# Kernel optimization log

Hardware: AMD Instinct MI355X
Metric: run time of the kernel (lower is better)

## Reference

```python
import jax, jax.numpy as jnp
import numpy as np

N_NODES = 100000
N_EDGES = 800000
C = 64        # in_channels == out_channels
H = 4         # num_heads
LN_EPS = 1e-5
SM_EPS = 1e-8


def setup_inputs() -> dict:
    key = jax.random.key(0)
    ks = jax.random.split(key, 8)
    return {
        "x": jax.random.normal(ks[0], (N_NODES, C), dtype=jnp.float32),
        "edge_index": jax.random.randint(ks[1], (2, N_EDGES), 0, N_NODES, dtype=jnp.int64),
        "edge_time": jax.random.uniform(ks[2], (N_EDGES,), dtype=jnp.float32),
        "current_time": 1,
        "W_w": jax.random.normal(ks[3], (C, C), dtype=jnp.float32) * (1.0 / np.sqrt(C)),
        "W_b": jnp.zeros((C,), dtype=jnp.float32),
        "attn_w": jax.random.normal(ks[4], (2 * C, H), dtype=jnp.float32) * (1.0 / np.sqrt(2 * C)),
        "attn_b": jnp.zeros((H,), dtype=jnp.float32),
        "decay_rate": jnp.full((1,), 0.1, dtype=jnp.float32),
        "proj_w": jax.random.normal(ks[5], (C * H, C), dtype=jnp.float32) * (1.0 / np.sqrt(C * H)),
        "proj_b": jnp.zeros((C,), dtype=jnp.float32),
        "ln_g": jnp.ones((C,), dtype=jnp.float32),
        "ln_b": jnp.zeros((C,), dtype=jnp.float32),
    }


def reference(x, edge_index, edge_time, current_time, W_w, W_b, attn_w, attn_b,
              decay_rate, proj_w, proj_b, ln_g, ln_b):
    num_nodes = x.shape[0]
    src, dst = edge_index[0], edge_index[1]

    # relation-specific transform (same Linear applied to src and dst node sets)
    h = x @ W_w + W_b                       # (N, C)
    h_src = h[src]                          # (E, C) gather
    h_dst = h[dst]                          # (E, C) gather

    # attention: Linear(2C -> H) + LeakyReLU(0.2)
    logits = h_src @ attn_w[:C] + h_dst @ attn_w[C:] + attn_b   # (E, H)
    scores = jax.nn.leaky_relu(logits, negative_slope=0.2)

    # temporal decay: exp(-softplus(lambda) * delta_t), multiplied pre-softmax
    delta_t = jnp.float32(current_time) - edge_time             # (E,)
    lam = jax.nn.softplus(decay_rate[0])
    scores = scores * jnp.exp(-lam * delta_t)[:, None]

    # segmented (per-destination) softmax over incoming edges
    smax = jax.ops.segment_max(scores, dst, num_segments=num_nodes)   # (N, H)
    e = jnp.exp(scores - smax[dst])                                   # (E, H)
    ssum = jax.ops.segment_sum(e, dst, num_segments=num_nodes)        # (N, H)
    attn = e / (ssum[dst] + SM_EPS)                                   # (E, H)

    # per-edge messages (E, C, H) -> (E, C*H), scatter-add to destinations
    msg = (h_src[:, :, None] * attn[:, None, :]).reshape(-1, C * H)
    agg = jax.ops.segment_sum(msg, dst, num_segments=num_nodes)       # (N, C*H)

    # single edge type -> mean over 1 message is identity
    out = agg @ proj_w + proj_b                                       # (N, C)
    # dropout p=0 (eval) -> identity; residual + LayerNorm + ReLU
    z = out + x
    mu = jnp.mean(z, axis=-1, keepdims=True)
    var = jnp.mean(jnp.square(z - mu), axis=-1, keepdims=True)
    y = ln_g * (z - mu) * jax.lax.rsqrt(var + LN_EPS) + ln_b
    return jax.nn.relu(y)
```

## Files before the change

### kernel.cpp

```cpp
#include <hip/hip_runtime.h>


typedef __attribute__((ext_vector_type(8))) short bf16x8;
typedef __attribute__((ext_vector_type(4))) float f32x4;

__device__ __forceinline__ unsigned short f2bf(float f) {
  unsigned int u = __float_as_uint(f);
  u += 0x7FFFu + ((u >> 16) & 1u);
  return (unsigned short)(u >> 16);
}
__device__ __forceinline__ float bf2f(unsigned short s) {
  return __uint_as_float(((unsigned int)s) << 16);
}

#define FMA4(P, S, R) { P.x = fmaf(S, R.x, P.x); P.y = fmaf(S, R.y, P.y); \
                        P.z = fmaf(S, R.z, P.z); P.w = fmaf(S, R.w, P.w); }

__global__ __launch_bounds__(64) void k_hn(const float* __restrict__ x,
    const float* __restrict__ Ww, const float* __restrict__ Wb,
    const float* __restrict__ attn_w,
    unsigned short* __restrict__ h16, float4* __restrict__ u,
    float4* __restrict__ v, int N)
{
  const int n = blockIdx.x * 64 + threadIdx.x;
  const bool valid = (n < N);
  const int nc = valid ? n : (N - 1);

  float o[64];
  #pragma unroll
  for (int c = 0; c < 64; ++c) o[c] = Wb[c];

  const float* xr = x + (size_t)nc * 64;
  for (int ch = 0; ch < 16; ++ch) {
    float4 xv = *(const float4*)(xr + ch * 4);
    float a[4] = {xv.x, xv.y, xv.z, xv.w};
    #pragma unroll
    for (int kk = 0; kk < 4; ++kk) {
      const float* Wr = Ww + (size_t)(ch * 4 + kk) * 64;
      #pragma unroll
      for (int c = 0; c < 64; ++c)
        o[c] = fmaf(a[kk], Wr[c], o[c]);
    }
  }

  float4 uu = make_float4(0.f, 0.f, 0.f, 0.f);
  float4 vv = make_float4(0.f, 0.f, 0.f, 0.f);
  const float4* aw = (const float4*)attn_w;
  #pragma unroll
  for (int c = 0; c < 64; ++c) {
    float4 r1 = aw[c];
    float4 r2 = aw[64 + c];
    FMA4(uu, o[c], r1);
    FMA4(vv, o[c], r2);
  }

  if (valid) {
    unsigned int* hr = (unsigned int*)(h16 + (size_t)n * 64);
    #pragma unroll
    for (int i = 0; i < 8; ++i) {
      uint4 w;
      w.x = (unsigned int)f2bf(o[i*8+0]) | ((unsigned int)f2bf(o[i*8+1]) << 16);
      w.y = (unsigned int)f2bf(o[i*8+2]) | ((unsigned int)f2bf(o[i*8+3]) << 16);
      w.z = (unsigned int)f2bf(o[i*8+4]) | ((unsigned int)f2bf(o[i*8+5]) << 16);
      w.w = (unsigned int)f2bf(o[i*8+6]) | ((unsigned int)f2bf(o[i*8+7]) << 16);
      *(uint4*)(hr + i * 4) = w;
    }
    u[n] = uu;
    v[n] = vv;
  }
}

__global__ __launch_bounds__(256) void k_score(const float4* __restrict__ u,
    const float4* __restrict__ v,
    const int* __restrict__ ei, const float* __restrict__ et,
    const int* __restrict__ ctime, const float* __restrict__ drate,
    const float* __restrict__ attn_b, float4* __restrict__ est,
    int* __restrict__ deg, int* __restrict__ rank, int E)
{
  int e = blockIdx.x * 256 + threadIdx.x;
  if (e >= E) return;
  const int src = ei[e];
  const int dst = ei[E + e];
  rank[e] = atomicAdd(&deg[dst], 1);
  const float4 us = u[src];
  const float4 vd = v[dst];
  const float4 ab = *(const float4*)attn_b;
  const float lam = log1pf(__expf(drate[0]));
  const float w = __expf(-lam * ((float)ctime[0] - et[e]));

  float4 o; float t;
  t = us.x + vd.x + ab.x; t = (t > 0.f ? t : 0.2f * t) * w; o.x = __expf(t);
  t = us.y + vd.y + ab.y; t = (t > 0.f ? t : 0.2f * t) * w; o.y = __expf(t);
  t = us.z + vd.z + ab.z; t = (t > 0.f ? t : 0.2f * t) * w; o.z = __expf(t);
  t = us.w + vd.w + ab.w; t = (t > 0.f ? t : 0.2f * t) * w; o.w = __expf(t);
  est[e] = o;
}

__global__ __launch_bounds__(256) void scan1(const int* __restrict__ deg,
    int* __restrict__ offs, int* __restrict__ bsums, int N)
{
  int i = blockIdx.x * 256 + threadIdx.x;
  int lane = threadIdx.x & 63;
  int w = threadIdx.x >> 6;
  int v = (i < N) ? deg[i] : 0;
  int s = v;
  #pragma unroll
  for (int d = 1; d < 64; d <<= 1) {
    int t = __shfl_up(s, d, 64);
    if (lane >= d) s += t;
  }
  __shared__ int wsum[4];
  if (lane == 63) wsum[w] = s;
  __syncthreads();
  int add = 0;
  if (w > 0) add += wsum[0];
  if (w > 1) add += wsum[1];
  if (w > 2) add += wsum[2];
  if (i < N) offs[i] = s - v + add;
  if (threadIdx.x == 255) bsums[blockIdx.x] = wsum[0] + wsum[1] + wsum[2] + wsum[3];
}

__global__ __launch_bounds__(512) void scan2(int* bsums, int NB)
{
  __shared__ int lds[512];
  int t = threadIdx.x;
  int v = (t < NB) ? bsums[t] : 0;
  lds[t] = v;
  __syncthreads();
  for (int s = 1; s < 512; s <<= 1) {
    int a = (t >= s) ? lds[t - s] : 0;
    __syncthreads();
    lds[t] += a;
    __syncthreads();
  }
  if (t < NB) bsums[t] = lds[t] - v;
}

__global__ __launch_bounds__(256) void k_fill(const int* __restrict__ ei,
    const int* __restrict__ offs, const int* __restrict__ bsums,
    const int* __restrict__ rank, const float4* __restrict__ est,
    int* __restrict__ csr_src, float4* __restrict__ csr_es, int E)
{
  int e = blockIdx.x * 256 + threadIdx.x;
  if (e >= E) return;
  int d = ei[E + e];
  int pos = offs[d] + bsums[d >> 8] + rank[e];
  csr_src[pos] = ei[e];
  csr_es[pos] = est[e];
}

__global__ __launch_bounds__(256) void k_agg(const unsigned short* __restrict__ h16,
    const int* __restrict__ csr_src, const float4* __restrict__ csr_es,
    const int* __restrict__ offs, const int* __restrict__ bsums,
    unsigned short* __restrict__ agg, int N, int E)
{
  const int c = threadIdx.x & 63;
  const int wid = blockIdx.x * 4 + (threadIdx.x >> 6);
  const int wstride = gridDim.x * 4;

  for (int n0 = wid; n0 < N; n0 += wstride) {
    const int n = __builtin_amdgcn_readfirstlane(n0);
    const int p0 = offs[n] + bsums[n >> 8];
    const int p1 = (n + 1 < N) ? (offs[n + 1] + bsums[(n + 1) >> 8]) : E;
    const int nf = (p1 - p0) & ~3;

    float acc0 = 0.f, acc1 = 0.f, acc2 = 0.f, acc3 = 0.f;
    float den0 = 0.f, den1 = 0.f, den2 = 0.f, den3 = 0.f;

    int4   sA = make_int4(0, 0, 0, 0);
    float4 eA0, eA1, eA2, eA3;
    float  gA0 = 0.f, gA1 = 0.f, gA2 = 0.f, gA3 = 0.f;
    if (nf) {
      sA = *(const int4*)(csr_src + p0);
      eA0 = csr_es[p0];     eA1 = csr_es[p0 + 1];
      eA2 = csr_es[p0 + 2]; eA3 = csr_es[p0 + 3];
      gA0 = bf2f(h16[(size_t)sA.x * 64 + c]);
      gA1 = bf2f(h16[(size_t)sA.y * 64 + c]);
      gA2 = bf2f(h16[(size_t)sA.z * 64 + c]);
      gA3 = bf2f(h16[(size_t)sA.w * 64 + c]);
    }
    for (int p = p0; p < p0 + nf; p += 4) {
      int4 sB; float4 eB0, eB1, eB2, eB3;
      float gB0, gB1, gB2, gB3;
      const bool more = (p + 4 < p0 + nf);
      if (more) {
        sB = *(const int4*)(csr_src + p + 4);
        eB0 = csr_es[p + 4]; eB1 = csr_es[p + 5];
        eB2 = csr_es[p + 6]; eB3 = csr_es[p + 7];
        gB0 = bf2f(h16[(size_t)sB.x * 64 + c]);
        gB1 = bf2f(h16[(size_t)sB.y * 64 + c]);
        gB2 = bf2f(h16[(size_t)sB.z * 64 + c]);
        gB3 = bf2f(h16[(size_t)sB.w * 64 + c]);
      }
      den0 += (eA0.x + eA1.x) + (eA2.x + eA3.x);
      den1 += (eA0.y + eA1.y) + (eA2.y + eA3.y);
      den2 += (eA0.z + eA1.z) + (eA2.z + eA3.z);
      den3 += (eA0.w + eA1.w) + (eA2.w + eA3.w);
      acc0 = fmaf(eA0.x, gA0, fmaf(eA1.x, gA1, fmaf(eA2.x, gA2, fmaf(eA3.x, gA3, acc0))));
      acc1 = fmaf(eA0.y, gA0, fmaf(eA1.y, gA1, fmaf(eA2.y, gA2, fmaf(eA3.y, gA3, acc1))));
      acc2 = fmaf(eA0.z, gA0, fmaf(eA1.z, gA1, fmaf(eA2.z, gA2, fmaf(eA3.z, gA3, acc2))));
      acc3 = fmaf(eA0.w, gA0, fmaf(eA1.w, gA1, fmaf(eA2.w, gA2, fmaf(eA3.w, gA3, acc3))));
      if (more) {
        eA0 = eB0; eA1 = eB1; eA2 = eB2; eA3 = eB3;
        gA0 = gB0; gA1 = gB1; gA2 = gB2; gA3 = gB3;
      }
    }
    for (int p = p0 + nf; p < p1; ++p) {
      int s = csr_src[p];
      float4 ev = csr_es[p];
      float g = bf2f(h16[(size_t)s * 64 + c]);
      den0 += ev.x; den1 += ev.y; den2 += ev.z; den3 += ev.w;
      acc0 = fmaf(ev.x, g, acc0);
      acc1 = fmaf(ev.y, g, acc1);
      acc2 = fmaf(ev.z, g, acc2);
      acc3 = fmaf(ev.w, g, acc3);
    }
    ushort4 o;
    o.x = f2bf(acc0 / (den0 + 1e-8f));
    o.y = f2bf(acc1 / (den1 + 1e-8f));
    o.z = f2bf(acc2 / (den2 + 1e-8f));
    o.w = f2bf(acc3 / (den3 + 1e-8f));
    *(ushort4*)(agg + (size_t)n * 256 + c * 4) = o;
  }
}

__global__ __launch_bounds__(256) void k_pw(const float* __restrict__ Pw,
    unsigned short* __restrict__ Bf)
{
  int i = blockIdx.x * 256 + threadIdx.x;
  int j    = i & 7;
  int lane = (i >> 3) & 63;
  int cb   = (i >> 9) & 3;
  int ks   = i >> 11;
  int k    = ks * 32 + (lane >> 4) * 8 + j;
  int colg = cb * 16 + (lane & 15);
  Bf[i] = f2bf(Pw[(size_t)k * 64 + colg]);
}

__global__ __launch_bounds__(256) void k_projm(const unsigned short* __restrict__ agg,
    const unsigned short* __restrict__ Bf, const float* __restrict__ x,
    const float* __restrict__ Pb,
    const float* __restrict__ lg, const float* __restrict__ lb,
    float* __restrict__ out, int N)
{
  const int lane = threadIdx.x & 63;
  const int wv = threadIdx.x >> 6;
  const int nt = blockIdx.x * 4 + wv;
  if (nt * 16 >= N) return;
  const int col  = lane & 15;
  const int quad = lane >> 4;
  const int base = nt * 16;

  int na = base + col; if (na >= N) na = N - 1;
  const unsigned short* aptr = agg + (size_t)na * 256 + quad * 8;

  f32x4 acc0 = {0.f, 0.f, 0.f, 0.f};
  f32x4 acc1 = {0.f, 0.f, 0.f, 0.f};
  f32x4 acc2 = {0.f, 0.f, 0.f, 0.f};
  f32x4 acc3 = {0.f, 0.f, 0.f, 0.f};

  #pragma unroll
  for (int ks = 0; ks < 8; ++ks) {
    bf16x8 av = *(const bf16x8*)(aptr + ks * 32);
    bf16x8 b0 = *(const bf16x8*)(Bf + ((size_t)(ks * 4 + 0) * 64 + lane) * 8);
    bf16x8 b1 = *(const bf16x8*)(Bf + ((size_t)(ks * 4 + 1) * 64 + lane) * 8);
    bf16x8 b2 = *(const bf16x8*)(Bf + ((size_t)(ks * 4 + 2) * 64 + lane) * 8);
    bf16x8 b3 = *(const bf16x8*)(Bf + ((size_t)(ks * 4 + 3) * 64 + lane) * 8);
    acc0 = __builtin_amdgcn_mfma_f32_16x16x32_bf16(av, b0, acc0, 0, 0, 0);
    acc1 = __builtin_amdgcn_mfma_f32_16x16x32_bf16(av, b1, acc1, 0, 0, 0);
    acc2 = __builtin_amdgcn_mfma_f32_16x16x32_bf16(av, b2, acc2, 0, 0, 0);
    acc3 = __builtin_amdgcn_mfma_f32_16x16x32_bf16(av, b3, acc3, 0, 0, 0);
  }

  const float pb0 = Pb[col], pb1 = Pb[16 + col], pb2 = Pb[32 + col], pb3 = Pb[48 + col];
  float v[4][4];
  #pragma unroll
  for (int r = 0; r < 4; ++r) {
    int node = base + quad * 4 + r; if (node >= N) node = N - 1;
    const float* xr = x + (size_t)node * 64;
    v[0][r] = acc0[r] + pb0 + xr[col];
    v[1][r] = acc1[r] + pb1 + xr[16 + col];
    v[2][r] = acc2[r] + pb2 + xr[32 + col];
    v[3][r] = acc3[r] + pb3 + xr[48 + col];
  }

  float mu[4], inv[4];
  #pragma unroll
  for (int r = 0; r < 4; ++r) {
    float s = (v[0][r] + v[1][r]) + (v[2][r] + v[3][r]);
    s += __shfl_xor(s, 1, 64); s += __shfl_xor(s, 2, 64);
    s += __shfl_xor(s, 4, 64); s += __shfl_xor(s, 8, 64);
    mu[r] = s * 0.015625f;
  }
  #pragma unroll
  for (int r = 0; r < 4; ++r) {
    float d0 = v[0][r] - mu[r], d1 = v[1][r] - mu[r];
    float d2 = v[2][r] - mu[r], d3 = v[3][r] - mu[r];
    float s = fmaf(d0, d0, d1 * d1) + fmaf(d2, d2, d3 * d3);
    s += __shfl_xor(s, 1, 64); s += __shfl_xor(s, 2, 64);
    s += __shfl_xor(s, 4, 64); s += __shfl_xor(s, 8, 64);
    inv[r] = rsqrtf(s * 0.015625f + 1e-5f);
  }

  const float lg0 = lg[col], lg1 = lg[16 + col], lg2 = lg[32 + col], lg3 = lg[48 + col];
  const float lb0 = lb[col], lb1 = lb[16 + col], lb2 = lb[32 + col], lb3 = lb[48 + col];
  #pragma unroll
  for (int r = 0; r < 4; ++r) {
    int node = base + quad * 4 + r;
    if (node < N) {
      float* orow = out + (size_t)node * 64;
      orow[col]      = fmaxf(fmaf(lg0 * (v[0][r] - mu[r]), inv[r], lb0), 0.f);
      orow[16 + col] = fmaxf(fmaf(lg1 * (v[1][r] - mu[r]), inv[r], lb1), 0.f);
      orow[32 + col] = fmaxf(fmaf(lg2 * (v[2][r] - mu[r]), inv[r], lb2), 0.f);
      orow[48 + col] = fmaxf(fmaf(lg3 * (v[3][r] - mu[r]), inv[r], lb3), 0.f);
    }
  }
}

extern "C" void kernel_launch(void* const* d_in, const int* in_sizes, int n_in,
                              void* d_out, int out_size, void* d_ws, size_t ws_size,
                              hipStream_t stream)
{
  const float* x  = (const float*)d_in[0];
  const int*   ei = (const int*)d_in[1];
  const float* et = (const float*)d_in[2];
  const int*   ct = (const int*)d_in[3];
  const float* Ww = (const float*)d_in[4];
  const float* Wb = (const float*)d_in[5];
  const float* aw = (const float*)d_in[6];
  const float* ab = (const float*)d_in[7];
  const float* dr = (const float*)d_in[8];
  const float* Pw = (const float*)d_in[9];
  const float* Pb = (const float*)d_in[10];
  const float* lg = (const float*)d_in[11];
  const float* lb = (const float*)d_in[12];
  float* out = (float*)d_out;

  const int N = in_sizes[0] / 64;
  const int E = in_sizes[2];

  char* ws = (char*)d_ws;
  size_t off = 0;
  auto take = [&](size_t bytes) -> char* {
    char* p = ws + off;
    off = (off + bytes + 255) & ~(size_t)255;
    return p;
  };
  unsigned short* h16 = (unsigned short*)take((size_t)N * 64 * 2);
  int*    deg    = (int*)take((size_t)N * 4);
  int*    offs   = (int*)take((size_t)N * 4);
  int*    bsums  = (int*)take(512 * 4);
  int*    rank   = (int*)take((size_t)E * 4);
  float4* est    = (float4*)take((size_t)E * 16);
  int*    csr_src= (int*)take((size_t)E * 4);
  float4* csr_es = (float4*)take((size_t)E * 16);
  unsigned short* agg = (unsigned short*)take((size_t)N * 256 * 2);
  float4* u      = (float4*)take((size_t)N * 16);
  float4* v      = (float4*)take((size_t)N * 16);
  unsigned short* Bf = (unsigned short*)take(16384 * 2);

  hipMemsetAsync(deg, 0, (size_t)N * 4, stream);

  k_pw<<<64, 256, 0, stream>>>(Pw, Bf);
  k_hn<<<(N + 63) / 64, 64, 0, stream>>>(x, Ww, Wb, aw, h16, u, v, N);
  k_score<<<(E + 255) / 256, 256, 0, stream>>>(u, v, ei, et, ct, dr, ab, est, deg, rank, E);
  const int NB = (N + 255) / 256;
  scan1<<<NB, 256, 0, stream>>>(deg, offs, bsums, N);
  scan2<<<1, 512, 0, stream>>>(bsums, NB);
  k_fill<<<(E + 255) / 256, 256, 0, stream>>>(ei, offs, bsums, rank, est, csr_src, csr_es, E);
  k_agg<<<2048, 256, 0, stream>>>(h16, csr_src, csr_es, offs, bsums, agg, N, E);
  const int NT = (N + 15) / 16;
  k_projm<<<(NT + 3) / 4, 256, 0, stream>>>(agg, Bf, x, Pb, lg, lb, out, N);
}
```

Before: 281.5 us.

## Fuse score computation into CSR fill and aggregation into projection+LayerNorm

Splits the old score kernel so a lightweight kernel only computes degrees and ranks. The edge-score computation moves into the CSR fill kernel, which removes the intermediate per-edge score buffer and its round trip through memory. The per-destination aggregation is fused with the MFMA projection, residual and LayerNorm: each block stages 16 aggregated rows in LDS as bf16, and the four waves then each compute 16 output columns, with LayerNorm statistics reduced through shared memory. This removes the N×256 bf16 agg buffer write and read, at the cost of a fixed one-node-per-wave mapping instead of grid-stride load balancing, plus extra barriers.

Result: slower. 322.8 us (+14.7%).

```diff
diff --git a/kernel.cpp b/kernel.cpp
--- a/kernel.cpp
+++ b/kernel.cpp
@@ -11,6 +11,9 @@
 }
 __device__ __forceinline__ float bf2f(unsigned short s) {
   return __uint_as_float(((unsigned int)s) << 16);
+}
+__device__ __forceinline__ unsigned int pk(float a, float b) {
+  return (unsigned int)f2bf(a) | ((unsigned int)f2bf(b) << 16);
 }
 
 #define FMA4(P, S, R) { P.x = fmaf(S, R.x, P.x); P.y = fmaf(S, R.y, P.y); \
@@ -59,10 +62,10 @@
     #pragma unroll
     for (int i = 0; i < 8; ++i) {
       uint4 w;
-      w.x = (unsigned int)f2bf(o[i*8+0]) | ((unsigned int)f2bf(o[i*8+1]) << 16);
-      w.y = (unsigned int)f2bf(o[i*8+2]) | ((unsigned int)f2bf(o[i*8+3]) << 16);
-      w.z = (unsigned int)f2bf(o[i*8+4]) | ((unsigned int)f2bf(o[i*8+5]) << 16);
-      w.w = (unsigned int)f2bf(o[i*8+6]) | ((unsigned int)f2bf(o[i*8+7]) << 16);
+      w.x = pk(o[i*8+0], o[i*8+1]);
+      w.y = pk(o[i*8+2], o[i*8+3]);
+      w.z = pk(o[i*8+4], o[i*8+5]);
+      w.w = pk(o[i*8+6], o[i*8+7]);
       *(uint4*)(hr + i * 4) = w;
     }
     u[n] = uu;
@@ -70,30 +73,11 @@
   }
 }
 
-__global__ __launch_bounds__(256) void k_score(const float4* __restrict__ u,
-    const float4* __restrict__ v,
-    const int* __restrict__ ei, const float* __restrict__ et,
-    const int* __restrict__ ctime, const float* __restrict__ drate,
-    const float* __restrict__ attn_b, float4* __restrict__ est,
+__global__ __launch_bounds__(256) void k_deg(const int* __restrict__ ei,
     int* __restrict__ deg, int* __restrict__ rank, int E)
 {
   int e = blockIdx.x * 256 + threadIdx.x;
-  if (e >= E) return;
-  const int src = ei[e];
-  const int dst = ei[E + e];
-  rank[e] = atomicAdd(&deg[dst], 1);
-  const float4 us = u[src];
-  const float4 vd = v[dst];
-  const float4 ab = *(const float4*)attn_b;
-  const float lam = log1pf(__expf(drate[0]));
-  const float w = __expf(-lam * ((float)ctime[0] - et[e]));
-
-  float4 o; float t;
-  t = us.x + vd.x + ab.x; t = (t > 0.f ? t : 0.2f * t) * w; o.x = __expf(t);
-  t = us.y + vd.y + ab.y; t = (t > 0.f ? t : 0.2f * t) * w; o.y = __expf(t);
-  t = us.z + vd.z + ab.z; t = (t > 0.f ? t : 0.2f * t) * w; o.z = __expf(t);
-  t = us.w + vd.w + ab.w; t = (t > 0.f ? t : 0.2f * t) * w; o.w = __expf(t);
-  est[e] = o;
+  if (e < E) rank[e] = atomicAdd(&deg[ei[E + e]], 1);
 }
 
 __global__ __launch_bounds__(256) void scan1(const int* __restrict__ deg,
@@ -137,91 +121,32 @@
 }
 
 __global__ __launch_bounds__(256) void k_fill(const int* __restrict__ ei,
+    const float* __restrict__ et, const int* __restrict__ ctime,
+    const float* __restrict__ drate, const float4* __restrict__ u,
+    const float4* __restrict__ v, const float* __restrict__ attn_b,
     const int* __restrict__ offs, const int* __restrict__ bsums,
-    const int* __restrict__ rank, const float4* __restrict__ est,
+    const int* __restrict__ rank,
     int* __restrict__ csr_src, float4* __restrict__ csr_es, int E)
 {
   int e = blockIdx.x * 256 + threadIdx.x;
   if (e >= E) return;
-  int d = ei[E + e];
-  int pos = offs[d] + bsums[d >> 8] + rank[e];
-  csr_src[pos] = ei[e];
-  csr_es[pos] = est[e];
-}
-
-__global__ __launch_bounds__(256) void k_agg(const unsigned short* __restrict__ h16,
-    const int* __restrict__ csr_src, const float4* __restrict__ csr_es,
-    const int* __restrict__ offs, const int* __restrict__ bsums,
-    unsigned short* __restrict__ agg, int N, int E)
-{
-  const int c = threadIdx.x & 63;
-  const int wid = blockIdx.x * 4 + (threadIdx.x >> 6);
-  const int wstride = gridDim.x * 4;
-
-  for (int n0 = wid; n0 < N; n0 += wstride) {
-    const int n = __builtin_amdgcn_readfirstlane(n0);
-    const int p0 = offs[n] + bsums[n >> 8];
-    const int p1 = (n + 1 < N) ? (offs[n + 1] + bsums[(n + 1) >> 8]) : E;
-    const int nf = (p1 - p0) & ~3;
-
-    float acc0 = 0.f, acc1 = 0.f, acc2 = 0.f, acc3 = 0.f;
-    float den0 = 0.f, den1 = 0.f, den2 = 0.f, den3 = 0.f;
-
-    int4   sA = make_int4(0, 0, 0, 0);
-    float4 eA0, eA1, eA2, eA3;
-    float  gA0 = 0.f, gA1 = 0.f, gA2 = 0.f, gA3 = 0.f;
-    if (nf) {
-      sA = *(const int4*)(csr_src + p0);
-      eA0 = csr_es[p0];     eA1 = csr_es[p0 + 1];
-      eA2 = csr_es[p0 + 2]; eA3 = csr_es[p0 + 3];
-      gA0 = bf2f(h16[(size_t)sA.x * 64 + c]);
-      gA1 = bf2f(h16[(size_t)sA.y * 64 + c]);
-      gA2 = bf2f(h16[(size_t)sA.z * 64 + c]);
-      gA3 = bf2f(h16[(size_t)sA.w * 64 + c]);
-    }
-    for (int p = p0; p < p0 + nf; p += 4) {
-      int4 sB; float4 eB0, eB1, eB2, eB3;
-      float gB0, gB1, gB2, gB3;
-      const bool more = (p + 4 < p0 + nf);
-      if (more) {
-        sB = *(const int4*)(csr_src + p + 4);
-        eB0 = csr_es[p + 4]; eB1 = csr_es[p + 5];
-        eB2 = csr_es[p + 6]; eB3 = csr_es[p + 7];
-        gB0 = bf2f(h16[(size_t)sB.x * 64 + c]);
-        gB1 = bf2f(h16[(size_t)sB.y * 64 + c]);
-        gB2 = bf2f(h16[(size_t)sB.z * 64 + c]);
-        gB3 = bf2f(h16[(size_t)sB.w * 64 + c]);
-      }
-      den0 += (eA0.x + eA1.x) + (eA2.x + eA3.x);
-      den1 += (eA0.y + eA1.y) + (eA2.y + eA3.y);
-      den2 += (eA0.z + eA1.z) + (eA2.z + eA3.z);
-      den3 += (eA0.w + eA1.w) + (eA2.w + eA3.w);
-      acc0 = fmaf(eA0.x, gA0, fmaf(eA1.x, gA1, fmaf(eA2.x, gA2, fmaf(eA3.x, gA3, acc0))));
-      acc1 = fmaf(eA0.y, gA0, fmaf(eA1.y, gA1, fmaf(eA2.y, gA2, fmaf(eA3.y, gA3, acc1))));
-      acc2 = fmaf(eA0.z, gA0, fmaf(eA1.z, gA1, fmaf(eA2.z, gA2, fmaf(eA3.z, gA3, acc2))));
-      acc3 = fmaf(eA0.w, gA0, fmaf(eA1.w, gA1, fmaf(eA2.w, gA2, fmaf(eA3.w, gA3, acc3))));
-      if (more) {
-        eA0 = eB0; eA1 = eB1; eA2 = eB2; eA3 = eB3;
-        gA0 = gB0; gA1 = gB1; gA2 = gB2; gA3 = gB3;
-      }
-    }
-    for (int p = p0 + nf; p < p1; ++p) {
-      int s = csr_src[p];
-      float4 ev = csr_es[p];
-      float g = bf2f(h16[(size_t)s * 64 + c]);
-      den0 += ev.x; den1 += ev.y; den2 += ev.z; den3 += ev.w;
-      acc0 = fmaf(ev.x, g, acc0);
-      acc1 = fmaf(ev.y, g, acc1);
-      acc2 = fmaf(ev.z, g, acc2);
-      acc3 = fmaf(ev.w, g, acc3);
-    }
-    ushort4 o;
-    o.x = f2bf(acc0 / (den0 + 1e-8f));
-    o.y = f2bf(acc1 / (den1 + 1e-8f));
-    o.z = f2bf(acc2 / (den2 + 1e-8f));
-    o.w = f2bf(acc3 / (den3 + 1e-8f));
-    *(ushort4*)(agg + (size_t)n * 256 + c * 4) = o;
-  }
+  const int s = ei[e];
+  const int d = ei[E + e];
+  const float4 us = u[s];
+  const float4 vd = v[d];
+  const float4 ab = *(const float4*)attn_b;
+  const float lam = log1pf(__expf(drate[0]));
+  const float w = __expf(-lam * ((float)ctime[0] - et[e]));
+
+  float4 o; float t;
+  t = us.x + vd.x + ab.x; t = (t > 0.f ? t : 0.2f * t) * w; o.x = __expf(t);
+  t = us.y + vd.y + ab.y; t = (t > 0.f ? t : 0.2f * t) * w; o.y = __expf(t);
+  t = us.z + vd.z + ab.z; t = (t > 0.f ? t : 0.2f * t) * w; o.z = __expf(t);
+  t = us.w + vd.w + ab.w; t = (t > 0.f ? t : 0.2f * t) * w; o.w = __expf(t);
+
+  const int pos = offs[d] + bsums[d >> 8] + rank[e];
+  csr_src[pos] = s;
+  csr_es[pos] = o;
 }
 
 __global__ __launch_bounds__(256) void k_pw(const float* __restrict__ Pw,
@@ -237,83 +162,126 @@
   Bf[i] = f2bf(Pw[(size_t)k * 64 + colg]);
 }
 
-__global__ __launch_bounds__(256) void k_projm(const unsigned short* __restrict__ agg,
-    const unsigned short* __restrict__ Bf, const float* __restrict__ x,
-    const float* __restrict__ Pb,
+__global__ __launch_bounds__(256) void k_aggproj(
+    const unsigned short* __restrict__ h16,
+    const int* __restrict__ csr_src, const float4* __restrict__ csr_es,
+    const int* __restrict__ offs, const int* __restrict__ bsums,
+    const unsigned short* __restrict__ Bf,
+    const float* __restrict__ x, const float* __restrict__ Pb,
     const float* __restrict__ lg, const float* __restrict__ lb,
-    float* __restrict__ out, int N)
-{
+    float* __restrict__ out, int N, int E)
+{
+  __shared__ unsigned short At[16][264];
+  __shared__ float S1[16][4], S2[16][4];
+
   const int lane = threadIdx.x & 63;
   const int wv = threadIdx.x >> 6;
-  const int nt = blockIdx.x * 4 + wv;
-  if (nt * 16 >= N) return;
-  const int col  = lane & 15;
-  const int quad = lane >> 4;
-  const int base = nt * 16;
-
-  int na = base + col; if (na >= N) na = N - 1;
-  const unsigned short* aptr = agg + (size_t)na * 256 + quad * 8;
-
-  f32x4 acc0 = {0.f, 0.f, 0.f, 0.f};
-  f32x4 acc1 = {0.f, 0.f, 0.f, 0.f};
-  f32x4 acc2 = {0.f, 0.f, 0.f, 0.f};
-  f32x4 acc3 = {0.f, 0.f, 0.f, 0.f};
-
+  const int base = blockIdx.x * 16;
+  const int c = lane;
+
+  for (int i = 0; i < 4; ++i) {
+    const int row = wv * 4 + i;
+    const int n = base + row;
+    float acc0 = 0.f, acc1 = 0.f, acc2 = 0.f, acc3 = 0.f;
+    float den0 = 0.f, den1 = 0.f, den2 = 0.f, den3 = 0.f;
+    if (n < N) {
+      const int p0 = offs[n] + bsums[n >> 8];
+      const int p1 = (n + 1 < N) ? (offs[n + 1] + bsums[(n + 1) >> 8]) : E;
+      const int nf = (p1 - p0) & ~3;
+
+      int4   sA = make_int4(0, 0, 0, 0);
+      float4 eA0, eA1, eA2, eA3;
+      float  gA0 = 0.f, gA1 = 0.f, gA2 = 0.f, gA3 = 0.f;
+      if (nf) {
+        sA = *(const int4*)(csr_src + p0);
+        eA0 = csr_es[p0];     eA1 = csr_es[p0 + 1];
+        eA2 = csr_es[p0 + 2]; eA3 = csr_es[p0 + 3];
+        gA0 = bf2f(h16[(size_t)sA.x * 64 + c]);
+        gA1 = bf2f(h16[(size_t)sA.y * 64 + c]);
+        gA2 = bf2f(h16[(size_t)sA.z * 64 + c]);
+        gA3 = bf2f(h16[(size_t)sA.w * 64 + c]);
+      }
+      for (int p = p0; p < p0 + nf; p += 4) {
+        int4 sB; float4 eB0, eB1, eB2, eB3;
+        float gB0, gB1, gB2, gB3;
+        const bool more = (p + 4 < p0 + nf);
+        if (more) {
+          sB = *(const int4*)(csr_src + p + 4);
+          eB0 = csr_es[p + 4]; eB1 = csr_es[p + 5];
+          eB2 = csr_es[p + 6]; eB3 = csr_es[p + 7];
+          gB0 = bf2f(h16[(size_t)sB.x * 64 + c]);
+          gB1 = bf2f(h16[(size_t)sB.y * 64 + c]);
+          gB2 = bf2f(h16[(size_t)sB.z * 64 + c]);
+          gB3 = bf2f(h16[(size_t)sB.w * 64 + c]);
+        }
+        den0 += (eA0.x + eA1.x) + (eA2.x + eA3.x);
+        den1 += (eA0.y + eA1.y) + (eA2.y + eA3.y);
+        den2 += (eA0.z + eA1.z) + (eA2.z + eA3.z);
+        den3 += (eA0.w + eA1.w) + (eA2.w + eA3.w);
+        acc0 = fmaf(eA0.x, gA0, fmaf(eA1.x, gA1, fmaf(eA2.x, gA2, fmaf(eA3.x, gA3, acc0))));
+        acc1 = fmaf(eA0.y, gA0, fmaf(eA1.y, gA1, fmaf(eA2.y, gA2, fmaf(eA3.y, gA3, acc1))));
+        acc2 = fmaf(eA0.z, gA0, fmaf(eA1.z, gA1, fmaf(eA2.z, gA2, fmaf(eA3.z, gA3, acc2))));
+        acc3 = fmaf(eA0.w, gA0, fmaf(eA1.w, gA1, fmaf(eA2.w, gA2, fmaf(eA3.w, gA3, acc3))));
+        if (more) {
+          eA0 = eB0; eA1 = eB1; eA2 = eB2; eA3 = eB3;
+          gA0 = gB0; gA1 = gB1; gA2 = gB2; gA3 = gB3;
+        }
+      }
+      for (int p = p0 + nf; p < p1; ++p) {
+        int s = csr_src[p];
+        float4 ev = csr_es[p];
+        float g = bf2f(h16[(size_t)s * 64 + c]);
+        den0 += ev.x; den1 += ev.y; den2 += ev.z; den3 += ev.w;
+        acc0 = fmaf(ev.x, g, acc0);
+        acc1 = fmaf(ev.y, g, acc1);
+        acc2 = fmaf(ev.z, g, acc2);
+        acc3 = fmaf(ev.w, g, acc3);
+      }
+    }
+    uint2 w;
+    w.x = pk(acc0 / (den0 + 1e-8f), acc1 / (den1 + 1e-8f));
+    w.y = pk(acc2 / (den2 + 1e-8f), acc3 / (den3 + 1e-8f));
+    *(uint2*)&At[row][c * 4] = w;
+  }
+  __syncthreads();
+
+  const int col = lane & 15, quad = lane >> 4;
+  f32x4 acc = {0.f, 0.f, 0.f, 0.f};
   #pragma unroll
   for (int ks = 0; ks < 8; ++ks) {
-    bf16x8 av = *(const bf16x8*)(aptr + ks * 32);
-    bf16x8 b0 = *(const bf16x8*)(Bf + ((size_t)(ks * 4 + 0) * 64 + lane) * 8);
-    bf16x8 b1 = *(const bf16x8*)(Bf + ((size_t)(ks * 4 + 1) * 64 + lane) * 8);
-    bf16x8 b2 = *(const bf16x8*)(Bf + ((size_t)(ks * 4 + 2) * 64 + lane) * 8);
-    bf16x8 b3 = *(const bf16x8*)(Bf + ((size_t)(ks * 4 + 3) * 64 + lane) * 8);
-    acc0 = __builtin_amdgcn_mfma_f32_16x16x32_bf16(av, b0, acc0, 0, 0, 0);
-    acc1 = __builtin_amdgcn_mfma_f32_16x16x32_bf16(av, b1, acc1, 0, 0, 0);
-    acc2 = __builtin_amdgcn_mfma_f32_16x16x32_bf16(av, b2, acc2, 0, 0, 0);
-    acc3 = __builtin_amdgcn_mfma_f32_16x16x32_bf16(av, b3, acc3, 0, 0, 0);
-  }
-
-  const float pb0 = Pb[col], pb1 = Pb[16 + col], pb2 = Pb[32 + col], pb3 = Pb[48 + col];
-  float v[4][4];
-  #pragma unroll
-  for (int r = 0; r < 4; ++r) {
-    int node = base + quad * 4 + r; if (node >= N) node = N - 1;
-    const float* xr = x + (size_t)node * 64;
-    v[0][r] = acc0[r] + pb0 + xr[col];
-    v[1][r] = acc1[r] + pb1 + xr[16 + col];
-    v[2][r] = acc2[r] + pb2 + xr[32 + col];
-    v[3][r] = acc3[r] + pb3 + xr[48 + col];
-  }
-
-  float mu[4], inv[4];
-  #pragma unroll
-  for (int r = 0; r < 4; ++r) {
-    float s = (v[0][r] + v[1][r]) + (v[2][r] + v[3][r]);
-    s += __shfl_xor(s, 1, 64); s += __shfl_xor(s, 2, 64);
-    s += __shfl_xor(s, 4, 64); s += __shfl_xor(s, 8, 64);
-    mu[r] = s * 0.015625f;
-  }
-  #pragma unroll
-  for (int r = 0; r < 4; ++r) {
-    float d0 = v[0][r] - mu[r], d1 = v[1][r] - mu[r];
-    float d2 = v[2][r] - mu[r], d3 = v[3][r] - mu[r];
-    float s = fmaf(d0, d0, d1 * d1) + fmaf(d2, d2, d3 * d3);
-    s += __shfl_xor(s, 1, 64); s += __shfl_xor(s, 2, 64);
-    s += __shfl_xor(s, 4, 64); s += __shfl_xor(s, 8, 64);
-    inv[r] = rsqrtf(s * 0.015625f + 1e-5f);
-  }
-
-  const float lg0 = lg[col], lg1 = lg[16 + col], lg2 = lg[32 + col], lg3 = lg[48 + col];
-  const float lb0 = lb[col], lb1 = lb[16 + col], lb2 = lb[32 + col], lb3 = lb[48 + col];
+    bf16x8 av = *(const bf16x8*)&At[lane & 15][ks * 32 + quad * 8];
+    bf16x8 bv = *(const bf16x8*)(Bf + ((size_t)(ks * 4 + wv) * 64 + lane) * 8);
+    acc = __builtin_amdgcn_mfma_f32_16x16x32_bf16(av, bv, acc, 0, 0, 0);
+  }
+
+  const int gcol = wv * 16 + col;
+  const float pb = Pb[gcol], gg = lg[gcol], bb = lb[gcol];
+  float z[4];
   #pragma unroll
   for (int r = 0; r < 4; ++r) {
     int node = base + quad * 4 + r;
-    if (node < N) {
-      float* orow = out + (size_t)node * 64;
-      orow[col]      = fmaxf(fmaf(lg0 * (v[0][r] - mu[r]), inv[r], lb0), 0.f);
-      orow[16 + col] = fmaxf(fmaf(lg1 * (v[1][r] - mu[r]), inv[r], lb1), 0.f);
-      orow[32 + col] = fmaxf(fmaf(lg2 * (v[2][r] - mu[r]), inv[r], lb2), 0.f);
-      orow[48 + col] = fmaxf(fmaf(lg3 * (v[3][r] - mu[r]), inv[r], lb3), 0.f);
-    }
+    int nn = node < N ? node : N - 1;
+    z[r] = acc[r] + pb + x[(size_t)nn * 64 + gcol];
+    float s1 = z[r], s2 = z[r] * z[r];
+    s1 += __shfl_xor(s1, 1, 64); s2 += __shfl_xor(s2, 1, 64);
+    s1 += __shfl_xor(s1, 2, 64); s2 += __shfl_xor(s2, 2, 64);
+    s1 += __shfl_xor(s1, 4, 64); s2 += __shfl_xor(s2, 4, 64);
+    s1 += __shfl_xor(s1, 8, 64); s2 += __shfl_xor(s2, 8, 64);
+    if (col == 0) { S1[quad * 4 + r][wv] = s1; S2[quad * 4 + r][wv] = s2; }
+  }
+  __syncthreads();
+
+  #pragma unroll
+  for (int r = 0; r < 4; ++r) {
+    const int ni = quad * 4 + r;
+    float sum1 = (S1[ni][0] + S1[ni][1]) + (S1[ni][2] + S1[ni][3]);
+    float sum2 = (S2[ni][0] + S2[ni][1]) + (S2[ni][2] + S2[ni][3]);
+    float mu = sum1 * 0.015625f;
+    float var = fmaf(-mu, mu, sum2 * 0.015625f);
+    float inv = rsqrtf(var + 1e-5f);
+    int node = base + ni;
+    if (node < N)
+      out[(size_t)node * 64 + gcol] = fmaxf(fmaf(gg * (z[r] - mu), inv, bb), 0.f);
   }
 }
 
@@ -351,10 +319,8 @@
   int*    offs   = (int*)take((size_t)N * 4);
   int*    bsums  = (int*)take(512 * 4);
   int*    rank   = (int*)take((size_t)E * 4);
-  float4* est    = (float4*)take((size_t)E * 16);
   int*    csr_src= (int*)take((size_t)E * 4);
   float4* csr_es = (float4*)take((size_t)E * 16);
-  unsigned short* agg = (unsigned short*)take((size_t)N * 256 * 2);
   float4* u      = (float4*)take((size_t)N * 16);
   float4* v      = (float4*)take((size_t)N * 16);
   unsigned short* Bf = (unsigned short*)take(16384 * 2);
@@ -363,12 +329,12 @@
 
   k_pw<<<64, 256, 0, stream>>>(Pw, Bf);
   k_hn<<<(N + 63) / 64, 64, 0, stream>>>(x, Ww, Wb, aw, h16, u, v, N);
-  k_score<<<(E + 255) / 256, 256, 0, stream>>>(u, v, ei, et, ct, dr, ab, est, deg, rank, E);
+  k_deg<<<(E + 255) / 256, 256, 0, stream>>>(ei, deg, rank, E);
   const int NB = (N + 255) / 256;
   scan1<<<NB, 256, 0, stream>>>(deg, offs, bsums, N);
   scan2<<<1, 512, 0, stream>>>(bsums, NB);
-  k_fill<<<(E + 255) / 256, 256, 0, stream>>>(ei, offs, bsums, rank, est, csr_src, csr_es, E);
-  k_agg<<<2048, 256, 0, stream>>>(h16, csr_src, csr_es, offs, bsums, agg, N, E);
-  const int NT = (N + 15) / 16;
-  k_projm<<<(NT + 3) / 4, 256, 0, stream>>>(agg, Bf, x, Pb, lg, lb, out, N);
-}
+  k_fill<<<(E + 255) / 256, 256, 0, stream>>>(ei, et, ct, dr, u, v, ab,
+                                              offs, bsums, rank, csr_src, csr_es, E);
+  k_aggproj<<<(N + 15) / 16, 256, 0, stream>>>(h16, csr_src, csr_es, offs, bsums,
+                                               Bf, x, Pb, lg, lb, out, N, E);
+}
```

## Fuse edge scoring into CSR fill and edge-balance aggregation across waves

Applied to the files above, without the earlier changes.

Edge score computation moves from the degree-count kernel into the CSR fill kernel, so the intermediate per-edge score buffer is no longer written and read back. A new small kernel materializes final CSR offsets once, so later kernels skip the offs+bsums addition. The aggregation kernel now splits edges evenly across waves and binary-searches node ranges, with a three-stage prefetch pipeline, instead of assigning whole nodes to waves. This is meant to balance load across skewed degrees and hide gather latency, at the cost of per-edge branchy node-boundary handling and extra index math.

Measured after the change: 319.7 us. +13.6%, slower.

```diff
diff --git a/kernel.cpp b/kernel.cpp
--- a/kernel.cpp
+++ b/kernel.cpp
@@ -11,6 +11,9 @@
 }
 __device__ __forceinline__ float bf2f(unsigned short s) {
   return __uint_as_float(((unsigned int)s) << 16);
+}
+__device__ __forceinline__ unsigned int pk(float a, float b) {
+  return (unsigned int)f2bf(a) | ((unsigned int)f2bf(b) << 16);
 }
 
 #define FMA4(P, S, R) { P.x = fmaf(S, R.x, P.x); P.y = fmaf(S, R.y, P.y); \
@@ -59,10 +62,10 @@
     #pragma unroll
     for (int i = 0; i < 8; ++i) {
       uint4 w;
-      w.x = (unsigned int)f2bf(o[i*8+0]) | ((unsigned int)f2bf(o[i*8+1]) << 16);
-      w.y = (unsigned int)f2bf(o[i*8+2]) | ((unsigned int)f2bf(o[i*8+3]) << 16);
-      w.z = (unsigned int)f2bf(o[i*8+4]) | ((unsigned int)f2bf(o[i*8+5]) << 16);
-      w.w = (unsigned int)f2bf(o[i*8+6]) | ((unsigned int)f2bf(o[i*8+7]) << 16);
+      w.x = pk(o[i*8+0], o[i*8+1]);
+      w.y = pk(o[i*8+2], o[i*8+3]);
+      w.z = pk(o[i*8+4], o[i*8+5]);
+      w.w = pk(o[i*8+6], o[i*8+7]);
       *(uint4*)(hr + i * 4) = w;
     }
     u[n] = uu;
@@ -70,30 +73,11 @@
   }
 }
 
-__global__ __launch_bounds__(256) void k_score(const float4* __restrict__ u,
-    const float4* __restrict__ v,
-    const int* __restrict__ ei, const float* __restrict__ et,
-    const int* __restrict__ ctime, const float* __restrict__ drate,
-    const float* __restrict__ attn_b, float4* __restrict__ est,
+__global__ __launch_bounds__(256) void k_deg(const int* __restrict__ ei,
     int* __restrict__ deg, int* __restrict__ rank, int E)
 {
   int e = blockIdx.x * 256 + threadIdx.x;
-  if (e >= E) return;
-  const int src = ei[e];
-  const int dst = ei[E + e];
-  rank[e] = atomicAdd(&deg[dst], 1);
-  const float4 us = u[src];
-  const float4 vd = v[dst];
-  const float4 ab = *(const float4*)attn_b;
-  const float lam = log1pf(__expf(drate[0]));
-  const float w = __expf(-lam * ((float)ctime[0] - et[e]));
-
-  float4 o; float t;
-  t = us.x + vd.x + ab.x; t = (t > 0.f ? t : 0.2f * t) * w; o.x = __expf(t);
-  t = us.y + vd.y + ab.y; t = (t > 0.f ? t : 0.2f * t) * w; o.y = __expf(t);
-  t = us.z + vd.z + ab.z; t = (t > 0.f ? t : 0.2f * t) * w; o.z = __expf(t);
-  t = us.w + vd.w + ab.w; t = (t > 0.f ? t : 0.2f * t) * w; o.w = __expf(t);
-  est[e] = o;
+  if (e < E) rank[e] = atomicAdd(&deg[ei[E + e]], 1);
 }
 
 __global__ __launch_bounds__(256) void scan1(const int* __restrict__ deg,
@@ -136,91 +120,118 @@
   if (t < NB) bsums[t] = lds[t] - v;
 }
 
+__global__ __launch_bounds__(256) void scan3(const int* __restrict__ offs,
+    const int* __restrict__ bsums, int* __restrict__ offs2, int N, int E)
+{
+  int i = blockIdx.x * 256 + threadIdx.x;
+  if (i < N) offs2[i] = offs[i] + bsums[i >> 8];
+  if (i == N) offs2[N] = E;
+}
+
 __global__ __launch_bounds__(256) void k_fill(const int* __restrict__ ei,
-    const int* __restrict__ offs, const int* __restrict__ bsums,
-    const int* __restrict__ rank, const float4* __restrict__ est,
+    const float* __restrict__ et, const int* __restrict__ ctime,
+    const float* __restrict__ drate, const float4* __restrict__ u,
+    const float4* __restrict__ v, const float* __restrict__ attn_b,
+    const int* __restrict__ offs2, const int* __restrict__ rank,
     int* __restrict__ csr_src, float4* __restrict__ csr_es, int E)
 {
   int e = blockIdx.x * 256 + threadIdx.x;
   if (e >= E) return;
-  int d = ei[E + e];
-  int pos = offs[d] + bsums[d >> 8] + rank[e];
-  csr_src[pos] = ei[e];
-  csr_es[pos] = est[e];
+  const int s = ei[e];
+  const int d = ei[E + e];
+  const float4 us = u[s];
+  const float4 vd = v[d];
+  const float4 ab = *(const float4*)attn_b;
+  const float lam = log1pf(__expf(drate[0]));
+  const float w = __expf(-lam * ((float)ctime[0] - et[e]));
+
+  float4 o; float t;
+  t = us.x + vd.x + ab.x; t = (t > 0.f ? t : 0.2f * t) * w; o.x = __expf(t);
+  t = us.y + vd.y + ab.y; t = (t > 0.f ? t : 0.2f * t) * w; o.y = __expf(t);
+  t = us.z + vd.z + ab.z; t = (t > 0.f ? t : 0.2f * t) * w; o.z = __expf(t);
+  t = us.w + vd.w + ab.w; t = (t > 0.f ? t : 0.2f * t) * w; o.w = __expf(t);
+
+  const int pos = offs2[d] + rank[e];
+  csr_src[pos] = s;
+  csr_es[pos] = o;
 }
 
 __global__ __launch_bounds__(256) void k_agg(const unsigned short* __restrict__ h16,
     const int* __restrict__ csr_src, const float4* __restrict__ csr_es,
-    const int* __restrict__ offs, const int* __restrict__ bsums,
-    unsigned short* __restrict__ agg, int N, int E)
+    const int* __restrict__ offs2, unsigned short* __restrict__ agg,
+    int N, int E, int W)
 {
   const int c = threadIdx.x & 63;
-  const int wid = blockIdx.x * 4 + (threadIdx.x >> 6);
-  const int wstride = gridDim.x * 4;
-
-  for (int n0 = wid; n0 < N; n0 += wstride) {
-    const int n = __builtin_amdgcn_readfirstlane(n0);
-    const int p0 = offs[n] + bsums[n >> 8];
-    const int p1 = (n + 1 < N) ? (offs[n + 1] + bsums[(n + 1) >> 8]) : E;
-    const int nf = (p1 - p0) & ~3;
-
-    float acc0 = 0.f, acc1 = 0.f, acc2 = 0.f, acc3 = 0.f;
-    float den0 = 0.f, den1 = 0.f, den2 = 0.f, den3 = 0.f;
-
-    int4   sA = make_int4(0, 0, 0, 0);
-    float4 eA0, eA1, eA2, eA3;
-    float  gA0 = 0.f, gA1 = 0.f, gA2 = 0.f, gA3 = 0.f;
-    if (nf) {
-      sA = *(const int4*)(csr_src + p0);
-      eA0 = csr_es[p0];     eA1 = csr_es[p0 + 1];
-      eA2 = csr_es[p0 + 2]; eA3 = csr_es[p0 + 3];
-      gA0 = bf2f(h16[(size_t)sA.x * 64 + c]);
-      gA1 = bf2f(h16[(size_t)sA.y * 64 + c]);
-      gA2 = bf2f(h16[(size_t)sA.z * 64 + c]);
-      gA3 = bf2f(h16[(size_t)sA.w * 64 + c]);
-    }
-    for (int p = p0; p < p0 + nf; p += 4) {
-      int4 sB; float4 eB0, eB1, eB2, eB3;
-      float gB0, gB1, gB2, gB3;
-      const bool more = (p + 4 < p0 + nf);
-      if (more) {
-        sB = *(const int4*)(csr_src + p + 4);
-        eB0 = csr_es[p + 4]; eB1 = csr_es[p + 5];
-        eB2 = csr_es[p + 6]; eB3 = csr_es[p + 7];
-        gB0 = bf2f(h16[(size_t)sB.x * 64 + c]);
-        gB1 = bf2f(h16[(size_t)sB.y * 64 + c]);
-        gB2 = bf2f(h16[(size_t)sB.z * 64 + c]);
-        gB3 = bf2f(h16[(size_t)sB.w * 64 + c]);
-      }
-      den0 += (eA0.x + eA1.x) + (eA2.x + eA3.x);
-      den1 += (eA0.y + eA1.y) + (eA2.y + eA3.y);
-      den2 += (eA0.z + eA1.z) + (eA2.z + eA3.z);
-      den3 += (eA0.w + eA1.w) + (eA2.w + eA3.w);
-      acc0 = fmaf(eA0.x, gA0, fmaf(eA1.x, gA1, fmaf(eA2.x, gA2, fmaf(eA3.x, gA3, acc0))));
-      acc1 = fmaf(eA0.y, gA0, fmaf(eA1.y, gA1, fmaf(eA2.y, gA2, fmaf(eA3.y, gA3, acc1))));
-      acc2 = fmaf(eA0.z, gA0, fmaf(eA1.z, gA1, fmaf(eA2.z, gA2, fmaf(eA3.z, gA3, acc2))));
-      acc3 = fmaf(eA0.w, gA0, fmaf(eA1.w, gA1, fmaf(eA2.w, gA2, fmaf(eA3.w, gA3, acc3))));
-      if (more) {
-        eA0 = eB0; eA1 = eB1; eA2 = eB2; eA3 = eB3;
-        gA0 = gB0; gA1 = gB1; gA2 = gB2; gA3 = gB3;
-      }
-    }
-    for (int p = p0 + nf; p < p1; ++p) {
-      int s = csr_src[p];
-      float4 ev = csr_es[p];
-      float g = bf2f(h16[(size_t)s * 64 + c]);
-      den0 += ev.x; den1 += ev.y; den2 += ev.z; den3 += ev.w;
-      acc0 = fmaf(ev.x, g, acc0);
-      acc1 = fmaf(ev.y, g, acc1);
-      acc2 = fmaf(ev.z, g, acc2);
-      acc3 = fmaf(ev.w, g, acc3);
-    }
-    ushort4 o;
-    o.x = f2bf(acc0 / (den0 + 1e-8f));
-    o.y = f2bf(acc1 / (den1 + 1e-8f));
-    o.z = f2bf(acc2 / (den2 + 1e-8f));
-    o.w = f2bf(acc3 / (den3 + 1e-8f));
-    *(ushort4*)(agg + (size_t)n * 256 + c * 4) = o;
+  const int wvid = blockIdx.x * 4 + (threadIdx.x >> 6);
+
+  const int eb = (int)((long)wvid * E / W);
+  const int ee = (int)((long)(wvid + 1) * E / W);
+
+  int lo = 0, hi = N;
+  while (lo < hi) { int m = (lo + hi) >> 1; if (offs2[m] >= eb) hi = m; else lo = m + 1; }
+  const int n0 = lo;
+  lo = 0; hi = N;
+  while (lo < hi) { int m = (lo + hi) >> 1; if (offs2[m] >= ee) hi = m; else lo = m + 1; }
+  int n1 = lo;
+  if (wvid == W - 1) n1 = N;
+  if (n0 >= n1) return;
+
+  int p = offs2[n0];
+  const int pendall = offs2[n1];
+  int n = n0;
+  int pe = offs2[n0 + 1];
+
+  float acc0 = 0.f, acc1 = 0.f, acc2 = 0.f, acc3 = 0.f;
+  float den0 = 0.f, den1 = 0.f, den2 = 0.f, den3 = 0.f;
+
+  auto flushNode = [&](int node) {
+    uint2 w;
+    w.x = pk(acc0 / (den0 + 1e-8f), acc1 / (den1 + 1e-8f));
+    w.y = pk(acc2 / (den2 + 1e-8f), acc3 / (den3 + 1e-8f));
+    *(uint2*)(agg + (size_t)node * 256 + c * 4) = w;
+    acc0 = acc1 = acc2 = acc3 = 0.f;
+    den0 = den1 = den2 = den3 = 0.f;
+  };
+  auto advance = [&](int q) {
+    while (pe == q) {
+      flushNode(n);
+      ++n;
+      if (n >= n1) { pe = -1; break; }
+      pe = offs2[n + 1];
+    }
+  };
+
+  float  gA[4], gB[4], gC[4];
+  float4 eA[4], eB[4], eC[4];
+  auto loadGroup = [&](int base, float* gg, float4* ee_) {
+    #pragma unroll
+    for (int j = 0; j < 4; ++j) {
+      int q = base + j < pendall ? base + j : pendall - 1;
+      int s = csr_src[q];
+      ee_[j] = csr_es[q];
+      gg[j] = bf2f(h16[(size_t)s * 64 + c]);
+    }
+  };
+
+  advance(p);
+  if (p < pendall) { loadGroup(p, gA, eA); loadGroup(p + 4, gB, eB); }
+
+  while (p < pendall) {
+    loadGroup(p + 8, gC, eC);
+    #pragma unroll
+    for (int j = 0; j < 4; ++j) {
+      if (p + j >= pendall) break;
+      den0 += eA[j].x; den1 += eA[j].y; den2 += eA[j].z; den3 += eA[j].w;
+      acc0 = fmaf(eA[j].x, gA[j], acc0);
+      acc1 = fmaf(eA[j].y, gA[j], acc1);
+      acc2 = fmaf(eA[j].z, gA[j], acc2);
+      acc3 = fmaf(eA[j].w, gA[j], acc3);
+      advance(p + j + 1);
+    }
+    p += 4;
+    #pragma unroll
+    for (int j = 0; j < 4; ++j) { gA[j] = gB[j]; eA[j] = eB[j];
+                                  gB[j] = gC[j]; eB[j] = eC[j]; }
   }
 }
 
@@ -349,9 +360,9 @@
   unsigned short* h16 = (unsigned short*)take((size_t)N * 64 * 2);
   int*    deg    = (int*)take((size_t)N * 4);
   int*    offs   = (int*)take((size_t)N * 4);
+  int*    offs2  = (int*)take((size_t)(N + 1) * 4);
   int*    bsums  = (int*)take(512 * 4);
   int*    rank   = (int*)take((size_t)E * 4);
-  float4* est    = (float4*)take((size_t)E * 16);
   int*    csr_src= (int*)take((size_t)E * 4);
   float4* csr_es = (float4*)take((size_t)E * 16);
   unsigned short* agg = (unsigned short*)take((size_t)N * 256 * 2);
@@ -363,12 +374,15 @@
 
   k_pw<<<64, 256, 0, stream>>>(Pw, Bf);
   k_hn<<<(N + 63) / 64, 64, 0, stream>>>(x, Ww, Wb, aw, h16, u, v, N);
-  k_score<<<(E + 255) / 256, 256, 0, stream>>>(u, v, ei, et, ct, dr, ab, est, deg, rank, E);
+  k_deg<<<(E + 255) / 256, 256, 0, stream>>>(ei, deg, rank, E);
   const int NB = (N + 255) / 256;
   scan1<<<NB, 256, 0, stream>>>(deg, offs, bsums, N);
   scan2<<<1, 512, 0, stream>>>(bsums, NB);
-  k_fill<<<(E + 255) / 256, 256, 0, stream>>>(ei, offs, bsums, rank, est, csr_src, csr_es, E);
-  k_agg<<<2048, 256, 0, stream>>>(h16, csr_src, csr_es, offs, bsums, agg, N, E);
+  scan3<<<NB + 1, 256, 0, stream>>>(offs, bsums, offs2, N, E);
+  k_fill<<<(E + 255) / 256, 256, 0, stream>>>(ei, et, ct, dr, u, v, ab,
+                                              offs2, rank, csr_src, csr_es, E);
+  const int W = 2048 * 4;
+  k_agg<<<2048, 256, 0, stream>>>(h16, csr_src, csr_es, offs2, agg, N, E, W);
   const int NT = (N + 15) / 16;
   k_projm<<<(NT + 3) / 4, 256, 0, stream>>>(agg, Bf, x, Pb, lg, lb, out, N);
 }
```
